# Optimization experiments

Measured on AMD Instinct MI355X. Metric: run time of the kernel, lower is better.

Reference implementation:

```python
import jax, jax.numpy as jnp
import numpy as np

N, IN_DIM, OUT_DIM, H = 50000, 128, 128, 4
C = OUT_DIM // H  # 32, per-head channels
E = 1_600_000
NEG_SLOPE = 0.2
LN_EPS = 1e-5


def setup_inputs() -> dict:
    key = jax.random.key(0)
    ks = jax.random.split(key, 12)
    x = jax.random.normal(ks[0], (N, IN_DIM), dtype=jnp.float32)
    edge_index = jax.random.randint(ks[1], (2, E), 0, N, dtype=jnp.int64)
    edge_weight = jax.random.uniform(ks[2], (E,), dtype=jnp.float32)
    s = 1.0 / np.sqrt(IN_DIM)
    W = jax.random.normal(ks[3], (IN_DIM, H * C), dtype=jnp.float32) * s
    att_src = jax.random.normal(ks[4], (1, H, C), dtype=jnp.float32) * s
    att_dst = jax.random.normal(ks[5], (1, H, C), dtype=jnp.float32) * s
    W_edge = jax.random.normal(ks[6], (1, H * C), dtype=jnp.float32)
    att_edge = jax.random.normal(ks[7], (1, H, C), dtype=jnp.float32) * s
    bias = jnp.zeros((H * C,), dtype=jnp.float32)
    ln_gamma = jnp.ones((OUT_DIM,), dtype=jnp.float32)
    ln_beta = jnp.zeros((OUT_DIM,), dtype=jnp.float32)
    return {"x": x, "edge_index": edge_index, "edge_weight": edge_weight,
            "W": W, "att_src": att_src, "att_dst": att_dst,
            "W_edge": W_edge, "att_edge": att_edge, "bias": bias,
            "ln_gamma": ln_gamma, "ln_beta": ln_beta}


def _gat_forward(x, edge_index, edge_weight, W, att_src, att_dst, W_edge, att_edge, bias):
    # GATConv(in, C, heads=H, edge_dim=1), concat=True, add_self_loops=True (fill_value='mean')
    xp = (x @ W).reshape(N, H, C)                      # [N,H,C]
    a_src = jnp.sum(xp * att_src, axis=-1)             # [N,H]
    a_dst = jnp.sum(xp * att_dst, axis=-1)             # [N,H]

    # add self-loops; self-loop edge_attr = mean of existing edge_attr
    loop = jnp.arange(N, dtype=edge_index.dtype)
    src = jnp.concatenate([edge_index[0], loop])       # [E+N]
    dst = jnp.concatenate([edge_index[1], loop])
    ew = jnp.concatenate([edge_weight, jnp.full((N,), jnp.mean(edge_weight), edge_weight.dtype)])

    ea = (ew[:, None] @ W_edge).reshape(-1, H, C)      # [E+N,H,C]
    a_edge = jnp.sum(ea * att_edge, axis=-1)           # [E+N,H]

    logits = a_src[src] + a_dst[dst] + a_edge          # [E+N,H]
    logits = jax.nn.leaky_relu(logits, NEG_SLOPE)

    # segment softmax over destination-node neighborhoods
    m = jax.ops.segment_max(logits, dst, num_segments=N)     # [N,H]
    ex = jnp.exp(logits - m[dst])
    denom = jax.ops.segment_sum(ex, dst, num_segments=N)     # [N,H]
    attn = ex / (denom[dst] + 1e-16)                          # [E+N,H]

    msg = attn[:, :, None] * xp[src]                          # [E+N,H,C]
    out = jax.ops.segment_sum(msg, dst, num_segments=N)      # [N,H,C]
    return out.reshape(N, H * C) + bias


def reference(x, edge_index, edge_weight, W, att_src, att_dst, W_edge, att_edge, bias, ln_gamma, ln_beta):
    out = _gat_forward(x, edge_index, edge_weight, W, att_src, att_dst, W_edge, att_edge, bias)
    # LayerNorm
    mu = jnp.mean(out, axis=-1, keepdims=True)
    var = jnp.mean(jnp.square(out - mu), axis=-1, keepdims=True)
    out = (out - mu) / jnp.sqrt(var + LN_EPS) * ln_gamma + ln_beta
    # ELU (dropout is identity in eval)
    return jax.nn.elu(out)
```

## Files before the change

### kernel.cpp

```cpp
#include <hip/hip_runtime.h>
#include <hip/hip_fp16.h>
#include <cstddef>

#define N_NODES 50000
#define E_EDGES 1600000
#define NEG_SLOPE 0.2f
#define LN_EPS 1e-5f
#define LOG2E 1.4426950408889634f
#define PAD 96

#define NBK 782
#define BCAP 2560
#define PCH 4096
#define NCH 391
#define NGB 1563
#define TPB 256

#define OFF_SCAL    0u
#define OFF_BCUR    256u
#define OFF_EWPART  4096u
#define OFF_COUNTS  8192u
#define OFF_ASRC    208256u
#define OFF_ADST    1008256u
#define OFF_XPH     1808256u
#define OFF_PAIRS   14608256u
#define OFF_STAGE   33808256u
#define OFF_WT      49823616u

#define XROW_B   272

typedef _Float16 half8 __attribute__((ext_vector_type(8)));
typedef float f32x4_t __attribute__((ext_vector_type(4)));

__device__ __forceinline__ float lrelu(float x) { return x > 0.f ? x : NEG_SLOPE * x; }

__device__ __forceinline__ float sel4(float4 v, int h) {
    float ab = (h & 1) ? v.y : v.x;
    float cd = (h & 1) ? v.w : v.z;
    return (h & 2) ? cd : ab;
}

__global__ __launch_bounds__(256) void k_w(const float* __restrict__ W,
                                           const float* __restrict__ W_edge,
                                           const float* __restrict__ att_edge,
                                           unsigned short* __restrict__ wt,
                                           float* __restrict__ scal) {
    int t = threadIdx.x;
    if (t < 128) {
        float p = W_edge[t] * att_edge[t];
        #pragma unroll
        for (int off = 16; off; off >>= 1) p += __shfl_down(p, off, 32);
        if ((t & 31) == 0) scal[4 + (t >> 5)] = p;
    }
    for (int i = t; i < 16384; i += 256) {
        int k = i >> 7, c = i & 127;
        wt[c * 128 + k] = __half_as_ushort(__float2half_rn(W[i]));
    }
}

__global__ __launch_bounds__(256, 4) void k_A(const float* __restrict__ x,
                                              const unsigned short* __restrict__ wt,
                                              const float* __restrict__ att_src, const float* __restrict__ att_dst,
                                              const int* __restrict__ ei, const float* __restrict__ ew,
                                              unsigned short* __restrict__ xph, float* __restrict__ a_src,
                                              float* __restrict__ a_dst, float* __restrict__ scal,
                                              int* __restrict__ bcur, uint2* __restrict__ staging,
                                              float* __restrict__ ewPart) {
    __shared__ __align__(16) char smem[16896];
    int t = threadIdx.x;

    if (blockIdx.x < NCH) {
        int* cnt   = (int*)smem;
        int* gbase = cnt + NBK;
        float* wred = (float*)(gbase + NBK);
        for (int i = t; i < NBK; i += 256) cnt[i] = 0;
        __syncthreads();

        int e0 = blockIdx.x * PCH;
        int lr[16];
        float s_ew = 0.f;
        #pragma unroll
        for (int i = 0; i < 16; i++) {
            int e = e0 + i * 256 + t;
            lr[i] = 0;
            if (e < E_EDGES) {
                int d = ei[E_EDGES + e];
                s_ew += ew[e];
                lr[i] = atomicAdd(&cnt[d >> 6], 1);
            }
        }
        #pragma unroll
        for (int off = 32; off; off >>= 1) s_ew += __shfl_down(s_ew, off, 64);
        if ((t & 63) == 0) wred[t >> 6] = s_ew;
        __syncthreads();
        if (t == 0) ewPart[blockIdx.x] = wred[0] + wred[1] + wred[2] + wred[3];
        for (int i = t; i < NBK; i += 256) gbase[i] = atomicAdd(&bcur[i], cnt[i]);
        __syncthreads();

        #pragma unroll
        for (int i = 0; i < 16; i++) {
            int e = e0 + i * 256 + t;
            if (e < E_EDGES) {
                int s = ei[e];
                int d = ei[E_EDGES + e];
                float w = ew[e];
                int b = d >> 6;
                uint2 ent;
                ent.x = (unsigned int)s |
                        ((unsigned int)__half_as_ushort(__float2half_rn(w)) << 16);
                ent.y = (unsigned int)d;
                staging[(size_t)b * BCAP + gbase[b] + lr[i]] = ent;
            }
        }
        return;
    }

    int gb = blockIdx.x - NCH;
    int r0 = gb * 32;

    for (int i = t; i < 1024; i += 256) {
        int row = i >> 5, c4 = i & 31;
        float4 v = make_float4(0.f, 0.f, 0.f, 0.f);
        if (r0 + row < N_NODES) v = ((const float4*)x)[(size_t)(r0 + row) * 32 + c4];
        __half2 h01 = __floats2half2_rn(v.x, v.y);
        __half2 h23 = __floats2half2_rn(v.z, v.w);
        uint2 pk;
        pk.x = *(unsigned int*)&h01;
        pk.y = *(unsigned int*)&h23;
        *(uint2*)(smem + XROW_B * row + 8 * c4) = pk;
    }
    __syncthreads();

    int lane = t & 63;
    int wv = t >> 6;
    int g = lane >> 4, q = lane & 15;
    int cb = 32 * wv;
    f32x4_t acc2[2][2] = {};
    {
        const char* pB = (const char*)wt;
        #pragma unroll
        for (int s = 0; s < 4; s++) {
            half8 a0 = *(const half8*)(smem + XROW_B * q + 64 * s + 16 * g);
            half8 a1 = *(const half8*)(smem + XROW_B * (16 + q) + 64 * s + 16 * g);
            half8 b0 = *(const half8*)(pB + (cb + q) * 256 + 64 * s + 16 * g);
            half8 b1 = *(const half8*)(pB + (cb + 16 + q) * 256 + 64 * s + 16 * g);
            acc2[0][0] = __builtin_amdgcn_mfma_f32_16x16x32_f16(a0, b0, acc2[0][0], 0, 0, 0);
            acc2[0][1] = __builtin_amdgcn_mfma_f32_16x16x32_f16(a0, b1, acc2[0][1], 0, 0, 0);
            acc2[1][0] = __builtin_amdgcn_mfma_f32_16x16x32_f16(a1, b0, acc2[1][0], 0, 0, 0);
            acc2[1][1] = __builtin_amdgcn_mfma_f32_16x16x32_f16(a1, b1, acc2[1][1], 0, 0, 0);
        }
    }
    __syncthreads();
    float* sxp = (float*)smem;
    {
        #pragma unroll
        for (int m = 0; m < 2; m++)
            #pragma unroll
            for (int nn = 0; nn < 2; nn++)
                #pragma unroll
                for (int r = 0; r < 4; r++)
                    sxp[(m * 16 + g * 4 + r) * 132 + cb + nn * 16 + q] = acc2[m][nn][r];
    }
    __syncthreads();

    int tc = t & 31;
    int tr = t >> 5;
    float4 s4 = ((const float4*)att_src)[tc];
    float4 d4 = ((const float4*)att_dst)[tc];
    int h = tc >> 3;
    #pragma unroll
    for (int r = 0; r < 4; r++) {
        int row = r0 + tr * 4 + r;
        if (row < N_NODES) {
            float4 a = ((const float4*)sxp)[(tr * 4 + r) * 33 + tc];
            __half2 h01 = __floats2half2_rn(a.x, a.y);
            __half2 h23 = __floats2half2_rn(a.z, a.w);
            uint2 pk;
            pk.x = *(unsigned int*)&h01;
            pk.y = *(unsigned int*)&h23;
            ((uint2*)xph)[(size_t)row * 32 + tc] = pk;
            float ps = a.x * s4.x + a.y * s4.y + a.z * s4.z + a.w * s4.w;
            float pd = a.x * d4.x + a.y * d4.y + a.z * d4.z + a.w * d4.w;
            ps += __shfl_down(ps, 4, 8); ps += __shfl_down(ps, 2, 8); ps += __shfl_down(ps, 1, 8);
            pd += __shfl_down(pd, 4, 8); pd += __shfl_down(pd, 2, 8); pd += __shfl_down(pd, 1, 8);
            if ((tc & 7) == 0) {
                a_src[(size_t)row * 4 + h] = ps;
                a_dst[(size_t)row * 4 + h] = pd;
            }
        }
    }
}

__global__ __launch_bounds__(256) void k_p2(const uint2* __restrict__ staging,
                                            const int* __restrict__ bcur,
                                            const float* __restrict__ ewPart,
                                            unsigned int* __restrict__ pairs,
                                            int* __restrict__ counts, float* __restrict__ scal) {
    int b = blockIdx.x, t = threadIdx.x;
    __shared__ int cnt2[64];
    __shared__ float wr2[4];
    if (b == 0) {
        float s = 0.f;
        for (int i = t; i < NCH; i += 256) s += ewPart[i];
        #pragma unroll
        for (int off = 32; off; off >>= 1) s += __shfl_down(s, off, 64);
        if ((t & 63) == 0) wr2[t >> 6] = s;
    }
    if (t < 64) cnt2[t] = 0;
    __syncthreads();
    if (b == 0 && t == 0) scal[0] = wr2[0] + wr2[1] + wr2[2] + wr2[3];
    int tot = bcur[b];
    const uint2* sg = staging + (size_t)b * BCAP;
    for (int i = t; i < tot; i += 256) {
        uint2 ent = sg[i];
        int d = (int)ent.y;
        int r = atomicAdd(&cnt2[d & 63], 1);
        pairs[(size_t)d * PAD + r] = ent.x;
    }
    __syncthreads();
    int n = (b << 6) + t;
    if (t < 64 && n < N_NODES) counts[n] = cnt2[t];
}

__global__ __launch_bounds__(256) void k_p3(const unsigned int* __restrict__ xpu,
                                            const float* __restrict__ a_src,
                                            const float* __restrict__ a_dst,
                                            const int* __restrict__ counts,
                                            const unsigned int* __restrict__ pairs,
                                            const float* __restrict__ scal,
                                            const float* __restrict__ bias,
                                            const float* __restrict__ gamma,
                                            const float* __restrict__ beta,
                                            float* __restrict__ out) {
    __shared__ unsigned long long sal[4][4][100];
    int lane = threadIdx.x & 63;
    int wv = threadIdx.x >> 6;
    int n = blockIdx.x * 4 + wv;
    if (n >= N_NODES) return;

    int h = lane >> 4;
    int em = lane & 15;

    float4 K = *(const float4*)(scal + 4);
    float Kh = sel4(K, h);
    float mean_ew = scal[0] * (1.0f / E_EDGES);

    int cnt = __builtin_amdgcn_readfirstlane(counts[n]);
    float4 ad4 = *(const float4*)(a_dst + (size_t)4 * n);
    float4 as4 = *(const float4*)(a_src + (size_t)4 * n);
    float adh = sel4(ad4, h);
    float aself = exp2f(lrelu(sel4(as4, h) + adh + Kh * mean_ew) * LOG2E);

    unsigned int pv = xpu[(size_t)n * 64 + lane];
    float2 f = __half22float2(*(__half2*)&pv);
    float acc0 = aself * f.x, acc1 = aself * f.y;

    unsigned long long* sl = &sal[wv][h][0];
    const unsigned int* prow = pairs + (size_t)n * PAD;
    float den = 0.f;
    #pragma unroll
    for (int b = 0; b < 6; b++) {
        if (b * 16 < cnt) {
            int e = b * 16 + em;
            float alpha = 0.f;
            int s = n;
            if (e < cnt) {
                unsigned int pk = prow[e];
                s = (int)(pk & 0xFFFFu);
                float w = __half2float(__ushort_as_half((unsigned short)(pk >> 16)));
                float4 av = *(const float4*)(a_src + (size_t)4 * s);
                alpha = exp2f(lrelu(sel4(av, h) + adh + Kh * w) * LOG2E);
            }
            den += alpha;
            sl[e] = ((unsigned long long)__float_as_uint(alpha) << 32) | (unsigned int)s;
        }
    }

    int cnt4 = (cnt + 3) & ~3;
    for (int e = 0; e < cnt4; e += 4) {
        ulonglong2 p01 = *(const ulonglong2*)(sl + e);
        ulonglong2 p23 = *(const ulonglong2*)(sl + e + 2);
        unsigned long long pq[4] = {p01.x, p01.y, p23.x, p23.y};
        #pragma unroll
        for (int q = 0; q < 4; q++) {
            unsigned int sj = (unsigned int)pq[q];
            float aj = __uint_as_float((unsigned int)(pq[q] >> 32));
            unsigned int g = xpu[(size_t)sj * 64 + lane];
            __half2 hh = *(__half2*)&g;
            acc0 = fmaf(aj, __half2float(__low2half(hh)), acc0);
            acc1 = fmaf(aj, __half2float(__high2half(hh)), acc1);
        }
    }

    den += __shfl_xor(den, 1, 64);
    den += __shfl_xor(den, 2, 64);
    den += __shfl_xor(den, 4, 64);
    den += __shfl_xor(den, 8, 64);
    den += aself;

    float inv = 1.0f / (den + 1e-16f);
    float2 b2 = ((const float2*)bias)[lane];
    float y0 = fmaf(acc0, inv, b2.x);
    float y1 = fmaf(acc1, inv, b2.y);

    float s1 = y0 + y1;
    #pragma unroll
    for (int off = 1; off < 64; off <<= 1) s1 += __shfl_xor(s1, off, 64);
    float mu = s1 * (1.f / 128.f);
    float d0 = y0 - mu, d1 = y1 - mu;
    float s2 = d0 * d0 + d1 * d1;
    #pragma unroll
    for (int off = 1; off < 64; off <<= 1) s2 += __shfl_xor(s2, off, 64);
    float rstd = rsqrtf(s2 * (1.f / 128.f) + LN_EPS);
    float2 g2 = ((const float2*)gamma)[lane];
    float2 be2 = ((const float2*)beta)[lane];
    float o0 = fmaf(d0 * rstd, g2.x, be2.x);
    float o1 = fmaf(d1 * rstd, g2.y, be2.y);
    o0 = o0 > 0.f ? o0 : expm1f(o0);
    o1 = o1 > 0.f ? o1 : expm1f(o1);
    float2 o; o.x = o0; o.y = o1;
    ((float2*)out)[(size_t)n * 64 + lane] = o;
}

extern "C" void kernel_launch(void* const* d_in, const int* in_sizes, int n_in,
                              void* d_out, int out_size, void* d_ws, size_t ws_size,
                              hipStream_t stream) {
    const float* x        = (const float*)d_in[0];
    const int*   ei       = (const int*)d_in[1];
    const float* ew       = (const float*)d_in[2];
    const float* W        = (const float*)d_in[3];
    const float* att_src  = (const float*)d_in[4];
    const float* att_dst  = (const float*)d_in[5];
    const float* W_edge   = (const float*)d_in[6];
    const float* att_edge = (const float*)d_in[7];
    const float* bias     = (const float*)d_in[8];
    const float* gamma    = (const float*)d_in[9];
    const float* beta     = (const float*)d_in[10];
    float* out = (float*)d_out;

    char* ws = (char*)d_ws;
    float* scal      = (float*)(ws + OFF_SCAL);
    int*   bcur      = (int*)(ws + OFF_BCUR);
    float* ewPart    = (float*)(ws + OFF_EWPART);
    int*   counts    = (int*)(ws + OFF_COUNTS);
    float* a_src     = (float*)(ws + OFF_ASRC);
    float* a_dst     = (float*)(ws + OFF_ADST);
    unsigned short* xph = (unsigned short*)(ws + OFF_XPH);
    unsigned int* pairs = (unsigned int*)(ws + OFF_PAIRS);
    uint2* staging   = (uint2*)(ws + OFF_STAGE);
    unsigned short* wt  = (unsigned short*)(ws + OFF_WT);

    hipMemsetAsync(bcur, 0, NBK * sizeof(int), stream);
    k_w<<<1, TPB, 0, stream>>>(W, W_edge, att_edge, wt, scal);
    k_A<<<NCH + NGB, TPB, 0, stream>>>(x, wt, att_src, att_dst, ei, ew,
                                       xph, a_src, a_dst, scal, bcur, staging, ewPart);
    k_p2<<<NBK, TPB, 0, stream>>>(staging, bcur, ewPart, pairs, counts, scal);
    k_p3<<<12500, TPB, 0, stream>>>((const unsigned int*)xph, a_src, a_dst, counts, pairs, scal,
                                    bias, gamma, beta, out);
}
```

Measured before the change: 236.3 us.

## Fuse bucket-to-node scatter into aggregation kernel via LDS with 16-node buckets

The separate k_p2 pass that scattered staged edges into a padded per-node pairs array in global memory is removed. Buckets shrink from 64 to 16 destination nodes, and k_p3 now loads each bucket's staged entries and sorts them by node in shared memory before the per-node softmax and aggregation. The memset of the bucket cursors and the edge-weight partial-sum reduction move into k_w and into atomics in k_A, which removes a launch and a global round trip. The cost is fewer aggregation blocks, each wave handling four nodes in sequence, plus more bucket counters in the partition pass.

```diff
diff --git a/kernel.cpp b/kernel.cpp
--- a/kernel.cpp
+++ b/kernel.cpp
@@ -9,8 +9,8 @@
 #define LOG2E 1.4426950408889634f
 #define PAD 96
 
-#define NBK 782
-#define BCAP 2560
+#define NBK 3125
+#define BCAP 704
 #define PCH 4096
 #define NCH 391
 #define NGB 1563
@@ -18,14 +18,11 @@
 
 #define OFF_SCAL    0u
 #define OFF_BCUR    256u
-#define OFF_EWPART  4096u
-#define OFF_COUNTS  8192u
 #define OFF_ASRC    208256u
 #define OFF_ADST    1008256u
 #define OFF_XPH     1808256u
-#define OFF_PAIRS   14608256u
-#define OFF_STAGE   33808256u
-#define OFF_WT      49823616u
+#define OFF_STAGE   14608256u
+#define OFF_WT      32208256u
 
 #define XROW_B   272
 
@@ -44,17 +41,23 @@
                                            const float* __restrict__ W_edge,
                                            const float* __restrict__ att_edge,
                                            unsigned short* __restrict__ wt,
-                                           float* __restrict__ scal) {
+                                           float* __restrict__ scal,
+                                           int* __restrict__ bcur) {
     int t = threadIdx.x;
-    if (t < 128) {
-        float p = W_edge[t] * att_edge[t];
-        #pragma unroll
-        for (int off = 16; off; off >>= 1) p += __shfl_down(p, off, 32);
-        if ((t & 31) == 0) scal[4 + (t >> 5)] = p;
-    }
-    for (int i = t; i < 16384; i += 256) {
-        int k = i >> 7, c = i & 127;
-        wt[c * 128 + k] = __half_as_ushort(__float2half_rn(W[i]));
+    int gid = blockIdx.x * 256 + t;
+    if (blockIdx.x == 0) {
+        if (t < 128) {
+            float p = W_edge[t] * att_edge[t];
+            #pragma unroll
+            for (int off = 16; off; off >>= 1) p += __shfl_down(p, off, 32);
+            if ((t & 31) == 0) scal[4 + (t >> 5)] = p;
+        }
+        if (t == 128) scal[0] = 0.f;
+    }
+    if (gid < NBK) bcur[gid] = 0;
+    if (gid < 16384) {
+        int k = gid >> 7, c = gid & 127;
+        wt[c * 128 + k] = __half_as_ushort(__float2half_rn(W[gid]));
     }
 }
 
@@ -64,15 +67,13 @@
                                               const int* __restrict__ ei, const float* __restrict__ ew,
                                               unsigned short* __restrict__ xph, float* __restrict__ a_src,
                                               float* __restrict__ a_dst, float* __restrict__ scal,
-                                              int* __restrict__ bcur, uint2* __restrict__ staging,
-                                              float* __restrict__ ewPart) {
-    __shared__ __align__(16) char smem[16896];
+                                              int* __restrict__ bcur, uint2* __restrict__ staging) {
+    __shared__ __align__(16) char smem[25088];
     int t = threadIdx.x;
 
     if (blockIdx.x < NCH) {
         int* cnt   = (int*)smem;
         int* gbase = cnt + NBK;
-        float* wred = (float*)(gbase + NBK);
         for (int i = t; i < NBK; i += 256) cnt[i] = 0;
         __syncthreads();
 
@@ -86,14 +87,13 @@
             if (e < E_EDGES) {
                 int d = ei[E_EDGES + e];
                 s_ew += ew[e];
-                lr[i] = atomicAdd(&cnt[d >> 6], 1);
+                lr[i] = atomicAdd(&cnt[d >> 4], 1);
             }
         }
         #pragma unroll
         for (int off = 32; off; off >>= 1) s_ew += __shfl_down(s_ew, off, 64);
-        if ((t & 63) == 0) wred[t >> 6] = s_ew;
         __syncthreads();
-        if (t == 0) ewPart[blockIdx.x] = wred[0] + wred[1] + wred[2] + wred[3];
+        if ((t & 63) == 0) atomicAdd(scal, s_ew);
         for (int i = t; i < NBK; i += 256) gbase[i] = atomicAdd(&bcur[i], cnt[i]);
         __syncthreads();
 
@@ -104,7 +104,7 @@
                 int s = ei[e];
                 int d = ei[E_EDGES + e];
                 float w = ew[e];
-                int b = d >> 6;
+                int b = d >> 4;
                 uint2 ent;
                 ent.x = (unsigned int)s |
                         ((unsigned int)__half_as_ushort(__float2half_rn(w)) << 16);
@@ -191,135 +191,122 @@
     }
 }
 
-__global__ __launch_bounds__(256) void k_p2(const uint2* __restrict__ staging,
-                                            const int* __restrict__ bcur,
-                                            const float* __restrict__ ewPart,
-                                            unsigned int* __restrict__ pairs,
-                                            int* __restrict__ counts, float* __restrict__ scal) {
-    int b = blockIdx.x, t = threadIdx.x;
-    __shared__ int cnt2[64];
-    __shared__ float wr2[4];
-    if (b == 0) {
-        float s = 0.f;
-        for (int i = t; i < NCH; i += 256) s += ewPart[i];
-        #pragma unroll
-        for (int off = 32; off; off >>= 1) s += __shfl_down(s, off, 64);
-        if ((t & 63) == 0) wr2[t >> 6] = s;
-    }
-    if (t < 64) cnt2[t] = 0;
-    __syncthreads();
-    if (b == 0 && t == 0) scal[0] = wr2[0] + wr2[1] + wr2[2] + wr2[3];
-    int tot = bcur[b];
-    const uint2* sg = staging + (size_t)b * BCAP;
-    for (int i = t; i < tot; i += 256) {
-        uint2 ent = sg[i];
-        int d = (int)ent.y;
-        int r = atomicAdd(&cnt2[d & 63], 1);
-        pairs[(size_t)d * PAD + r] = ent.x;
-    }
-    __syncthreads();
-    int n = (b << 6) + t;
-    if (t < 64 && n < N_NODES) counts[n] = cnt2[t];
-}
-
 __global__ __launch_bounds__(256) void k_p3(const unsigned int* __restrict__ xpu,
                                             const float* __restrict__ a_src,
                                             const float* __restrict__ a_dst,
-                                            const int* __restrict__ counts,
-                                            const unsigned int* __restrict__ pairs,
+                                            const uint2* __restrict__ staging,
+                                            const int* __restrict__ bcur,
                                             const float* __restrict__ scal,
                                             const float* __restrict__ bias,
                                             const float* __restrict__ gamma,
                                             const float* __restrict__ beta,
                                             float* __restrict__ out) {
+    __shared__ unsigned int pl[16][100];
+    __shared__ int lcnt[16];
     __shared__ unsigned long long sal[4][4][100];
-    int lane = threadIdx.x & 63;
-    int wv = threadIdx.x >> 6;
-    int n = blockIdx.x * 4 + wv;
-    if (n >= N_NODES) return;
-
+    int b = blockIdx.x;
+    int t = threadIdx.x;
+
+    if (t < 16) lcnt[t] = 0;
+    __syncthreads();
+    int tot = bcur[b];
+    const uint2* sg = staging + (size_t)b * BCAP;
+    for (int i = t; i < tot; i += 256) {
+        uint2 ent = sg[i];
+        int dl = (int)ent.y & 15;
+        int r = atomicAdd(&lcnt[dl], 1);
+        pl[dl][r] = ent.x;
+    }
+    __syncthreads();
+
+    int lane = t & 63;
+    int wv = t >> 6;
     int h = lane >> 4;
     int em = lane & 15;
 
     float4 K = *(const float4*)(scal + 4);
     float Kh = sel4(K, h);
     float mean_ew = scal[0] * (1.0f / E_EDGES);
-
-    int cnt = __builtin_amdgcn_readfirstlane(counts[n]);
-    float4 ad4 = *(const float4*)(a_dst + (size_t)4 * n);
-    float4 as4 = *(const float4*)(a_src + (size_t)4 * n);
-    float adh = sel4(ad4, h);
-    float aself = exp2f(lrelu(sel4(as4, h) + adh + Kh * mean_ew) * LOG2E);
-
-    unsigned int pv = xpu[(size_t)n * 64 + lane];
-    float2 f = __half22float2(*(__half2*)&pv);
-    float acc0 = aself * f.x, acc1 = aself * f.y;
-
     unsigned long long* sl = &sal[wv][h][0];
-    const unsigned int* prow = pairs + (size_t)n * PAD;
-    float den = 0.f;
-    #pragma unroll
-    for (int b = 0; b < 6; b++) {
-        if (b * 16 < cnt) {
-            int e = b * 16 + em;
-            float alpha = 0.f;
-            int s = n;
-            if (e < cnt) {
-                unsigned int pk = prow[e];
-                s = (int)(pk & 0xFFFFu);
-                float w = __half2float(__ushort_as_half((unsigned short)(pk >> 16)));
-                float4 av = *(const float4*)(a_src + (size_t)4 * s);
-                alpha = exp2f(lrelu(sel4(av, h) + adh + Kh * w) * LOG2E);
-            }
-            den += alpha;
-            sl[e] = ((unsigned long long)__float_as_uint(alpha) << 32) | (unsigned int)s;
-        }
-    }
-
-    int cnt4 = (cnt + 3) & ~3;
-    for (int e = 0; e < cnt4; e += 4) {
-        ulonglong2 p01 = *(const ulonglong2*)(sl + e);
-        ulonglong2 p23 = *(const ulonglong2*)(sl + e + 2);
-        unsigned long long pq[4] = {p01.x, p01.y, p23.x, p23.y};
-        #pragma unroll
-        for (int q = 0; q < 4; q++) {
-            unsigned int sj = (unsigned int)pq[q];
-            float aj = __uint_as_float((unsigned int)(pq[q] >> 32));
-            unsigned int g = xpu[(size_t)sj * 64 + lane];
-            __half2 hh = *(__half2*)&g;
-            acc0 = fmaf(aj, __half2float(__low2half(hh)), acc0);
-            acc1 = fmaf(aj, __half2float(__high2half(hh)), acc1);
-        }
-    }
-
-    den += __shfl_xor(den, 1, 64);
-    den += __shfl_xor(den, 2, 64);
-    den += __shfl_xor(den, 4, 64);
-    den += __shfl_xor(den, 8, 64);
-    den += aself;
-
-    float inv = 1.0f / (den + 1e-16f);
-    float2 b2 = ((const float2*)bias)[lane];
-    float y0 = fmaf(acc0, inv, b2.x);
-    float y1 = fmaf(acc1, inv, b2.y);
-
-    float s1 = y0 + y1;
-    #pragma unroll
-    for (int off = 1; off < 64; off <<= 1) s1 += __shfl_xor(s1, off, 64);
-    float mu = s1 * (1.f / 128.f);
-    float d0 = y0 - mu, d1 = y1 - mu;
-    float s2 = d0 * d0 + d1 * d1;
-    #pragma unroll
-    for (int off = 1; off < 64; off <<= 1) s2 += __shfl_xor(s2, off, 64);
-    float rstd = rsqrtf(s2 * (1.f / 128.f) + LN_EPS);
-    float2 g2 = ((const float2*)gamma)[lane];
-    float2 be2 = ((const float2*)beta)[lane];
-    float o0 = fmaf(d0 * rstd, g2.x, be2.x);
-    float o1 = fmaf(d1 * rstd, g2.y, be2.y);
-    o0 = o0 > 0.f ? o0 : expm1f(o0);
-    o1 = o1 > 0.f ? o1 : expm1f(o1);
-    float2 o; o.x = o0; o.y = o1;
-    ((float2*)out)[(size_t)n * 64 + lane] = o;
+
+    for (int j = 0; j < 4; j++) {
+        int nl = (wv << 2) + j;
+        int n = (b << 4) + nl;
+        int cnt = __builtin_amdgcn_readfirstlane(lcnt[nl]);
+
+        float4 ad4 = *(const float4*)(a_dst + (size_t)4 * n);
+        float4 as4 = *(const float4*)(a_src + (size_t)4 * n);
+        float adh = sel4(ad4, h);
+        float aself = exp2f(lrelu(sel4(as4, h) + adh + Kh * mean_ew) * LOG2E);
+
+        unsigned int pv = xpu[(size_t)n * 64 + lane];
+        float2 f = __half22float2(*(__half2*)&pv);
+        float acc0 = aself * f.x, acc1 = aself * f.y;
+
+        float den = 0.f;
+        #pragma unroll
+        for (int bb = 0; bb < 6; bb++) {
+            if (bb * 16 < cnt) {
+                int e = bb * 16 + em;
+                float alpha = 0.f;
+                int s = n;
+                if (e < cnt) {
+                    unsigned int pk = pl[nl][e];
+                    s = (int)(pk & 0xFFFFu);
+                    float w = __half2float(__ushort_as_half((unsigned short)(pk >> 16)));
+                    float4 av = *(const float4*)(a_src + (size_t)4 * s);
+                    alpha = exp2f(lrelu(sel4(av, h) + adh + Kh * w) * LOG2E);
+                }
+                den += alpha;
+                sl[e] = ((unsigned long long)__float_as_uint(alpha) << 32) | (unsigned int)s;
+            }
+        }
+
+        int cnt4 = (cnt + 3) & ~3;
+        for (int e = 0; e < cnt4; e += 4) {
+            ulonglong2 p01 = *(const ulonglong2*)(sl + e);
+            ulonglong2 p23 = *(const ulonglong2*)(sl + e + 2);
+            unsigned long long pq[4] = {p01.x, p01.y, p23.x, p23.y};
+            #pragma unroll
+            for (int q = 0; q < 4; q++) {
+                unsigned int sj = (unsigned int)pq[q];
+                float aj = __uint_as_float((unsigned int)(pq[q] >> 32));
+                unsigned int g = xpu[(size_t)sj * 64 + lane];
+                __half2 hh = *(__half2*)&g;
+                acc0 = fmaf(aj, __half2float(__low2half(hh)), acc0);
+                acc1 = fmaf(aj, __half2float(__high2half(hh)), acc1);
+            }
+        }
+
+        den += __shfl_xor(den, 1, 64);
+        den += __shfl_xor(den, 2, 64);
+        den += __shfl_xor(den, 4, 64);
+        den += __shfl_xor(den, 8, 64);
+        den += aself;
+
+        float inv = 1.0f / (den + 1e-16f);
+        float2 b2 = ((const float2*)bias)[lane];
+        float y0 = fmaf(acc0, inv, b2.x);
+        float y1 = fmaf(acc1, inv, b2.y);
+
+        float s1 = y0 + y1;
+        #pragma unroll
+        for (int off = 1; off < 64; off <<= 1) s1 += __shfl_xor(s1, off, 64);
+        float mu = s1 * (1.f / 128.f);
+        float d0 = y0 - mu, d1 = y1 - mu;
+        float s2 = d0 * d0 + d1 * d1;
+        #pragma unroll
+        for (int off = 1; off < 64; off <<= 1) s2 += __shfl_xor(s2, off, 64);
+        float rstd = rsqrtf(s2 * (1.f / 128.f) + LN_EPS);
+        float2 g2 = ((const float2*)gamma)[lane];
+        float2 be2 = ((const float2*)beta)[lane];
+        float o0 = fmaf(d0 * rstd, g2.x, be2.x);
+        float o1 = fmaf(d1 * rstd, g2.y, be2.y);
+        o0 = o0 > 0.f ? o0 : expm1f(o0);
+        o1 = o1 > 0.f ? o1 : expm1f(o1);
+        float2 o; o.x = o0; o.y = o1;
+        ((float2*)out)[(size_t)n * 64 + lane] = o;
+    }
 }
 
 extern "C" void kernel_launch(void* const* d_in, const int* in_sizes, int n_in,
@@ -341,20 +328,15 @@
     char* ws = (char*)d_ws;
     float* scal      = (float*)(ws + OFF_SCAL);
     int*   bcur      = (int*)(ws + OFF_BCUR);
-    float* ewPart    = (float*)(ws + OFF_EWPART);
-    int*   counts    = (int*)(ws + OFF_COUNTS);
     float* a_src     = (float*)(ws + OFF_ASRC);
     float* a_dst     = (float*)(ws + OFF_ADST);
     unsigned short* xph = (unsigned short*)(ws + OFF_XPH);
-    unsigned int* pairs = (unsigned int*)(ws + OFF_PAIRS);
     uint2* staging   = (uint2*)(ws + OFF_STAGE);
     unsigned short* wt  = (unsigned short*)(ws + OFF_WT);
 
-    hipMemsetAsync(bcur, 0, NBK * sizeof(int), stream);
-    k_w<<<1, TPB, 0, stream>>>(W, W_edge, att_edge, wt, scal);
+    k_w<<<64, TPB, 0, stream>>>(W, W_edge, att_edge, wt, scal, bcur);
     k_A<<<NCH + NGB, TPB, 0, stream>>>(x, wt, att_src, att_dst, ei, ew,
-                                       xph, a_src, a_dst, scal, bcur, staging, ewPart);
-    k_p2<<<NBK, TPB, 0, stream>>>(staging, bcur, ewPart, pairs, counts, scal);
-    k_p3<<<12500, TPB, 0, stream>>>((const unsigned int*)xph, a_src, a_dst, counts, pairs, scal,
-                                    bias, gamma, beta, out);
-}
+                                       xph, a_src, a_dst, scal, bcur, staging);
+    k_p3<<<NBK, TPB, 0, stream>>>((const unsigned int*)xph, a_src, a_dst, staging, bcur, scal,
+                                  bias, gamma, beta, out);
+}
```

Result: faster. 222.2 us (-6.0%).
